# Performance work log

Hardware: AMD Instinct MI355X
Metric: run time of the kernel (lower is better)

The kernel has to match this reference:

```python
import jax, jax.numpy as jnp
import numpy as np


def setup_inputs() -> dict:
    key = jax.random.key(0)
    ks = jax.random.split(key, 10)
    N, CZ, CH = 512, 128, 128
    s = 1.0 / np.sqrt(CZ)  # keep pre-sigmoid activations in a sane range
    return {
        "z": jax.random.normal(ks[0], (N, N, CZ), dtype=jnp.float32),
        "mask": jnp.ones((N, N, 1), dtype=jnp.float32),
        "weight_ag": jax.random.normal(ks[1], (CH, CZ), dtype=jnp.float32) * s,
        "bias_ag": jax.random.normal(ks[2], (CH,), dtype=jnp.float32) * 0.02,
        "weight_ap": jax.random.normal(ks[3], (CH, CZ), dtype=jnp.float32) * s,
        "bias_ap": jax.random.normal(ks[4], (CH,), dtype=jnp.float32) * 0.02,
        "weight_bg": jax.random.normal(ks[5], (CH, CZ), dtype=jnp.float32) * s,
        "bias_bg": jax.random.normal(ks[6], (CH,), dtype=jnp.float32) * 0.02,
        "weight_bp": jax.random.normal(ks[7], (CH, CZ), dtype=jnp.float32) * s,
        "bias_bp": jax.random.normal(ks[8], (CH,), dtype=jnp.float32) * 0.02,
        "chunk_size": 32,
    }


def _triangle_mul(z, mask, w_ag, b_ag, w_ap, b_ap, w_bg, b_bg, w_bp, b_bp):
    # z: [N, N, c_z]; mask: [N, N, 1]; weights: [c, c_z]
    # a = mask * sigmoid(Linear_ag(z)) * Linear_ap(z)   -> [N, N, c]
    a = mask * jax.nn.sigmoid(jnp.einsum("ijz,cz->ijc", z, w_ag) + b_ag) * (
        jnp.einsum("ijz,cz->ijc", z, w_ap) + b_ap
    )
    b = mask * jax.nn.sigmoid(jnp.einsum("ijz,cz->ijc", z, w_bg) + b_bg) * (
        jnp.einsum("ijz,cz->ijc", z, w_bp) + b_bp
    )
    # outgoing triangle multiplicative combination, channel-first output [c, N, N]
    return jnp.einsum("ikc,jkc->cij", a, b)


def reference(z, mask, weight_ag, bias_ag, weight_ap, bias_ap,
              weight_bg, bias_bg, weight_bp, bias_bp, chunk_size):
    # The torch wrapper chunks the hidden-channel dim of the weights and
    # concatenates the per-chunk [c, N, N] outputs along dim 0. Since every
    # channel is independent, this is mathematically identical to running the
    # full computation at once; we do that (clean, fused form).
    return _triangle_mul(z, mask, weight_ag, bias_ag, weight_ap, bias_ap,
                         weight_bg, bias_bg, weight_bp, bias_bp)
```

## Files before the change

kernel.cpp:

```cpp
#include <hip/hip_runtime.h>
#include <stdint.h>


#define NDIM 512
#define CZ   128
#define CH   128
#define NPOS (NDIM * NDIM)
#define TILES 4

typedef __attribute__((ext_vector_type(8))) __bf16 bf16x8;
typedef __attribute__((ext_vector_type(4))) float  f32x4;

__device__ __forceinline__ unsigned short f2bf(float f) {
  unsigned int u = __builtin_bit_cast(unsigned int, f);
  unsigned int r = (u + 0x7fffu + ((u >> 16) & 1u)) >> 16;
  return (unsigned short)r;
}

__global__ __launch_bounds__(256) void conv_weights(
    const float* __restrict__ wag, const float* __restrict__ wap,
    const float* __restrict__ wbg, const float* __restrict__ wbp,
    unsigned short* __restrict__ wbf) {
  int idx = blockIdx.x * 256 + threadIdx.x;
  int proj = idx >> 14;
  int rem  = idx & 16383;
  const float* src = (proj == 0) ? wag : (proj == 1) ? wap : (proj == 2) ? wbg : wbp;
  wbf[idx] = f2bf(src[rem]);
}

__global__ __launch_bounds__(256, 2) void proj_fuse(
    const float* __restrict__ z,
    const float* __restrict__ mask,
    const unsigned short* __restrict__ wbf,
    const float* __restrict__ bias_ag, const float* __restrict__ bias_ap,
    const float* __restrict__ bias_bg, const float* __restrict__ bias_bp,
    unsigned short* __restrict__ a_ws,
    unsigned short* __restrict__ b_ws) {
  __shared__ unsigned short zbuf[64 * 136];
  __shared__ unsigned short tbuf[128 * 72];

  const int t    = threadIdx.x;
  const int lane = t & 63;
  const int wave = t >> 6;
  const int wm   = wave >> 1;
  const int wn   = wave & 1;
  const int pair = blockIdx.y;
  const int pg   = pair * 2, pp = pg + 1;

  const int mrow  = wm * 32 + (lane & 15);
  const int nrow  = wn * 64 + (lane & 15);
  const int koffl = (lane >> 4) * 8;

  bf16x8 wg[4][4], wp[4][4];
#pragma unroll
  for (int ks = 0; ks < 4; ++ks)
#pragma unroll
    for (int ni = 0; ni < 4; ++ni) {
      const int c = nrow + ni * 16;
      wg[ks][ni] = *(const bf16x8*)&wbf[(pg * CH + c) * CZ + ks * 32 + koffl];
      wp[ks][ni] = *(const bf16x8*)&wbf[(pp * CH + c) * CZ + ks * 32 + koffl];
    }

  const float* bgp = pair ? bias_bg : bias_ag;
  const float* bpp = pair ? bias_bp : bias_ap;
  unsigned short* plane = pair ? b_ws : a_ws;

  const int col4  = t & 31;
  const int rbase = t >> 5;

  const int m0 = blockIdx.x * (TILES * 64);

  float4 zf[8];
#pragma unroll
  for (int it = 0; it < 8; ++it)
    zf[it] = *(const float4*)(z + (size_t)(m0 + it * 8 + rbase) * CZ + col4 * 4);

  for (int tt = 0; tt < TILES; ++tt) {
    const int mt = m0 + tt * 64;

#pragma unroll
    for (int it = 0; it < 8; ++it) {
      const int row = it * 8 + rbase;
      unsigned int lo = (unsigned int)f2bf(zf[it].x) | ((unsigned int)f2bf(zf[it].y) << 16);
      unsigned int hi = (unsigned int)f2bf(zf[it].z) | ((unsigned int)f2bf(zf[it].w) << 16);
      *(uint2*)&zbuf[row * 136 + col4 * 4] = make_uint2(lo, hi);
    }
    __syncthreads();

    if (tt + 1 < TILES) {
#pragma unroll
      for (int it = 0; it < 8; ++it)
        zf[it] = *(const float4*)(z + (size_t)(mt + 64 + it * 8 + rbase) * CZ + col4 * 4);
    }
    float mk[2][4];
#pragma unroll
    for (int mi = 0; mi < 2; ++mi)
#pragma unroll
      for (int r = 0; r < 4; ++r)
        mk[mi][r] = mask[mt + wm * 32 + mi * 16 + (lane >> 4) * 4 + r];

    f32x4 accg[2][4], accp[2][4];
#pragma unroll
    for (int mi = 0; mi < 2; ++mi)
#pragma unroll
      for (int ni = 0; ni < 4; ++ni) {
        accg[mi][ni] = (f32x4){0.f, 0.f, 0.f, 0.f};
        accp[mi][ni] = (f32x4){0.f, 0.f, 0.f, 0.f};
      }
#pragma unroll
    for (int ks = 0; ks < 4; ++ks) {
      bf16x8 af0 = *(const bf16x8*)&zbuf[(mrow)      * 136 + ks * 32 + koffl];
      bf16x8 af1 = *(const bf16x8*)&zbuf[(mrow + 16) * 136 + ks * 32 + koffl];
#pragma unroll
      for (int ni = 0; ni < 4; ++ni) {
        accg[0][ni] = __builtin_amdgcn_mfma_f32_16x16x32_bf16(af0, wg[ks][ni], accg[0][ni], 0, 0, 0);
        accg[1][ni] = __builtin_amdgcn_mfma_f32_16x16x32_bf16(af1, wg[ks][ni], accg[1][ni], 0, 0, 0);
        accp[0][ni] = __builtin_amdgcn_mfma_f32_16x16x32_bf16(af0, wp[ks][ni], accp[0][ni], 0, 0, 0);
        accp[1][ni] = __builtin_amdgcn_mfma_f32_16x16x32_bf16(af1, wp[ks][ni], accp[1][ni], 0, 0, 0);
      }
    }

#pragma unroll
    for (int ni = 0; ni < 4; ++ni) {
      const int c = nrow + ni * 16;
      const float bgv = bgp[c];
      const float bpv = bpp[c];
#pragma unroll
      for (int mi = 0; mi < 2; ++mi) {
        unsigned short h[4];
#pragma unroll
        for (int r = 0; r < 4; ++r) {
          float g = accg[mi][ni][r] + bgv;
          float p = accp[mi][ni][r] + bpv;
          float s = 1.0f / (1.0f + __expf(-g));
          h[r] = f2bf(mk[mi][r] * s * p);
        }
        const int mloc = wm * 32 + mi * 16 + (lane >> 4) * 4;
        *(uint2*)&tbuf[c * 72 + mloc] =
            make_uint2((unsigned int)h[0] | ((unsigned int)h[1] << 16),
                       (unsigned int)h[2] | ((unsigned int)h[3] << 16));
      }
    }
    __syncthreads();

    {
      const int p4 = t & 15;
      const int cb = t >> 4;
#pragma unroll
      for (int it = 0; it < 8; ++it) {
        const int c = it * 16 + cb;
        uint2 v = *(const uint2*)&tbuf[c * 72 + p4 * 4];
        *(uint2*)(plane + (size_t)c * NPOS + mt + p4 * 4) = v;
      }
    }
  }
}

__global__ __launch_bounds__(256, 3) void tri_gemm(
    const unsigned short* __restrict__ a_ws,
    const unsigned short* __restrict__ b_ws,
    float* __restrict__ out) {
  __shared__ unsigned short sA[128 * 64];
  __shared__ unsigned short sB[128 * 64];

  const int t = threadIdx.x, lane = t & 63, wave = t >> 6;
  const int wm = wave >> 1, wn = wave & 1;
  const int tj = blockIdx.x, ti = blockIdx.y, c = blockIdx.z;
  const int i0 = ti * 128, j0 = tj * 128;

  const unsigned short* Ap = a_ws + (size_t)c * NPOS + (size_t)i0 * NDIM;
  const unsigned short* Bp = b_ws + (size_t)c * NPOS + (size_t)j0 * NDIM;

  f32x4 acc[4][4];
#pragma unroll
  for (int mi = 0; mi < 4; ++mi)
#pragma unroll
    for (int ni = 0; ni < 4; ++ni) acc[mi][ni] = (f32x4){0.f, 0.f, 0.f, 0.f};

  const int srow8  = t >> 3;
  const int schunk = t & 7;
  const int mrow = wm * 64 + (lane & 15);
  const int nrow = wn * 64 + (lane & 15);

  for (int kk = 0; kk < 8; ++kk) {
    const int k0 = kk * 64;
#pragma unroll
    for (int i = 0; i < 4; ++i) {
      const int row = i * 32 + srow8;
      const int kcs = schunk ^ (row & 7);
      __builtin_amdgcn_global_load_lds(
          (const __attribute__((address_space(1))) unsigned int*)(Ap + (size_t)row * NDIM + k0 + kcs * 8),
          (__attribute__((address_space(3))) unsigned int*)&sA[(i * 256 + t) * 8], 16, 0, 0);
      __builtin_amdgcn_global_load_lds(
          (const __attribute__((address_space(1))) unsigned int*)(Bp + (size_t)row * NDIM + k0 + kcs * 8),
          (__attribute__((address_space(3))) unsigned int*)&sB[(i * 256 + t) * 8], 16, 0, 0);
    }
    __syncthreads();

#pragma unroll
    for (int ksub = 0; ksub < 2; ++ksub) {
      const int kc = ksub * 4 + (lane >> 4);
      bf16x8 af[4], bfr[4];
#pragma unroll
      for (int mi = 0; mi < 4; ++mi) {
        const int r = mrow + mi * 16;
        af[mi] = *(const bf16x8*)&sA[r * 64 + ((kc ^ (r & 7)) << 3)];
      }
#pragma unroll
      for (int ni = 0; ni < 4; ++ni) {
        const int r = nrow + ni * 16;
        bfr[ni] = *(const bf16x8*)&sB[r * 64 + ((kc ^ (r & 7)) << 3)];
      }
#pragma unroll
      for (int mi = 0; mi < 4; ++mi)
#pragma unroll
        for (int ni = 0; ni < 4; ++ni)
          acc[mi][ni] = __builtin_amdgcn_mfma_f32_16x16x32_bf16(af[mi], bfr[ni], acc[mi][ni], 0, 0, 0);
    }
    __syncthreads();
  }

  float* O = out + (size_t)c * NPOS + (size_t)i0 * NDIM + j0;
#pragma unroll
  for (int mi = 0; mi < 4; ++mi)
#pragma unroll
    for (int r = 0; r < 4; ++r) {
      const int m = wm * 64 + mi * 16 + (lane >> 4) * 4 + r;
#pragma unroll
      for (int ni = 0; ni < 4; ++ni) {
        const int n = wn * 64 + ni * 16 + (lane & 15);
        O[(size_t)m * NDIM + n] = acc[mi][ni][r];
      }
    }
}

extern "C" void kernel_launch(void* const* d_in, const int* in_sizes, int n_in,
                              void* d_out, int out_size, void* d_ws, size_t ws_size,
                              hipStream_t stream) {
  const float* z    = (const float*)d_in[0];
  const float* mask = (const float*)d_in[1];
  const float* wag  = (const float*)d_in[2];
  const float* bag  = (const float*)d_in[3];
  const float* wap  = (const float*)d_in[4];
  const float* bap  = (const float*)d_in[5];
  const float* wbg  = (const float*)d_in[6];
  const float* bbg  = (const float*)d_in[7];
  const float* wbp  = (const float*)d_in[8];
  const float* bbp  = (const float*)d_in[9];
  float* out = (float*)d_out;

  unsigned short* wbf  = (unsigned short*)d_ws;
  unsigned short* a_ws = (unsigned short*)((char*)d_ws + 131072);
  unsigned short* b_ws = (unsigned short*)((char*)d_ws + 131072 + (size_t)CH * NPOS * 2);

  conv_weights<<<dim3(256), dim3(256), 0, stream>>>(wag, wap, wbg, wbp, wbf);
  proj_fuse<<<dim3(NPOS / (64 * TILES), 2), dim3(256), 0, stream>>>(
      z, mask, wbf, bag, bap, bbg, bbp, a_ws, b_ws);
  tri_gemm<<<dim3(4, 4, CH), dim3(256), 0, stream>>>(a_ws, b_ws, out);
}
```

Before: 435.0 us.

## Restructure projection kernel: one block computes all four projections for 32 positions

```diff
diff --git a/kernel.cpp b/kernel.cpp
--- a/kernel.cpp
+++ b/kernel.cpp
@@ -6,7 +6,6 @@
 #define CZ   128
 #define CH   128
 #define NPOS (NDIM * NDIM)
-#define TILES 4
 
 typedef __attribute__((ext_vector_type(8))) __bf16 bf16x8;
 typedef __attribute__((ext_vector_type(4))) float  f32x4;
@@ -15,6 +14,12 @@
   unsigned int u = __builtin_bit_cast(unsigned int, f);
   unsigned int r = (u + 0x7fffu + ((u >> 16) & 1u)) >> 16;
   return (unsigned short)r;
+}
+__device__ __forceinline__ float bf2f_lo(unsigned int u) {
+  return __builtin_bit_cast(float, u << 16);
+}
+__device__ __forceinline__ float bf2f_hi(unsigned int u) {
+  return __builtin_bit_cast(float, u & 0xffff0000u);
 }
 
 __global__ __launch_bounds__(256) void conv_weights(
@@ -28,7 +33,7 @@
   wbf[idx] = f2bf(src[rem]);
 }
 
-__global__ __launch_bounds__(256, 2) void proj_fuse(
+__global__ __launch_bounds__(256, 3) void proj_fuse(
     const float* __restrict__ z,
     const float* __restrict__ mask,
     const unsigned short* __restrict__ wbf,
@@ -36,122 +41,95 @@
     const float* __restrict__ bias_bg, const float* __restrict__ bias_bp,
     unsigned short* __restrict__ a_ws,
     unsigned short* __restrict__ b_ws) {
-  __shared__ unsigned short zbuf[64 * 136];
-  __shared__ unsigned short tbuf[128 * 72];
+  __shared__ unsigned short zbuf[32 * 136];
+  __shared__ unsigned short accb[4 * 128 * 36];
 
   const int t    = threadIdx.x;
   const int lane = t & 63;
-  const int wave = t >> 6;
-  const int wm   = wave >> 1;
-  const int wn   = wave & 1;
-  const int pair = blockIdx.y;
-  const int pg   = pair * 2, pp = pg + 1;
-
-  const int mrow  = wm * 32 + (lane & 15);
-  const int nrow  = wn * 64 + (lane & 15);
-  const int koffl = (lane >> 4) * 8;
-
-  bf16x8 wg[4][4], wp[4][4];
-#pragma unroll
-  for (int ks = 0; ks < 4; ++ks)
-#pragma unroll
-    for (int ni = 0; ni < 4; ++ni) {
-      const int c = nrow + ni * 16;
-      wg[ks][ni] = *(const bf16x8*)&wbf[(pg * CH + c) * CZ + ks * 32 + koffl];
-      wp[ks][ni] = *(const bf16x8*)&wbf[(pp * CH + c) * CZ + ks * 32 + koffl];
-    }
-
-  const float* bgp = pair ? bias_bg : bias_ag;
-  const float* bpp = pair ? bias_bp : bias_ap;
-  unsigned short* plane = pair ? b_ws : a_ws;
-
-  const int col4  = t & 31;
-  const int rbase = t >> 5;
-
-  const int m0 = blockIdx.x * (TILES * 64);
-
-  float4 zf[8];
-#pragma unroll
-  for (int it = 0; it < 8; ++it)
-    zf[it] = *(const float4*)(z + (size_t)(m0 + it * 8 + rbase) * CZ + col4 * 4);
-
-  for (int tt = 0; tt < TILES; ++tt) {
-    const int mt = m0 + tt * 64;
-
-#pragma unroll
-    for (int it = 0; it < 8; ++it) {
-      const int row = it * 8 + rbase;
-      unsigned int lo = (unsigned int)f2bf(zf[it].x) | ((unsigned int)f2bf(zf[it].y) << 16);
-      unsigned int hi = (unsigned int)f2bf(zf[it].z) | ((unsigned int)f2bf(zf[it].w) << 16);
-      *(uint2*)&zbuf[row * 136 + col4 * 4] = make_uint2(lo, hi);
-    }
-    __syncthreads();
-
-    if (tt + 1 < TILES) {
-#pragma unroll
-      for (int it = 0; it < 8; ++it)
-        zf[it] = *(const float4*)(z + (size_t)(mt + 64 + it * 8 + rbase) * CZ + col4 * 4);
-    }
-    float mk[2][4];
-#pragma unroll
-    for (int mi = 0; mi < 2; ++mi)
-#pragma unroll
-      for (int r = 0; r < 4; ++r)
-        mk[mi][r] = mask[mt + wm * 32 + mi * 16 + (lane >> 4) * 4 + r];
-
-    f32x4 accg[2][4], accp[2][4];
-#pragma unroll
-    for (int mi = 0; mi < 2; ++mi)
-#pragma unroll
-      for (int ni = 0; ni < 4; ++ni) {
-        accg[mi][ni] = (f32x4){0.f, 0.f, 0.f, 0.f};
-        accp[mi][ni] = (f32x4){0.f, 0.f, 0.f, 0.f};
-      }
-#pragma unroll
-    for (int ks = 0; ks < 4; ++ks) {
-      bf16x8 af0 = *(const bf16x8*)&zbuf[(mrow)      * 136 + ks * 32 + koffl];
-      bf16x8 af1 = *(const bf16x8*)&zbuf[(mrow + 16) * 136 + ks * 32 + koffl];
-#pragma unroll
-      for (int ni = 0; ni < 4; ++ni) {
-        accg[0][ni] = __builtin_amdgcn_mfma_f32_16x16x32_bf16(af0, wg[ks][ni], accg[0][ni], 0, 0, 0);
-        accg[1][ni] = __builtin_amdgcn_mfma_f32_16x16x32_bf16(af1, wg[ks][ni], accg[1][ni], 0, 0, 0);
-        accp[0][ni] = __builtin_amdgcn_mfma_f32_16x16x32_bf16(af0, wp[ks][ni], accp[0][ni], 0, 0, 0);
-        accp[1][ni] = __builtin_amdgcn_mfma_f32_16x16x32_bf16(af1, wp[ks][ni], accp[1][ni], 0, 0, 0);
-      }
-    }
-
-#pragma unroll
-    for (int ni = 0; ni < 4; ++ni) {
-      const int c = nrow + ni * 16;
-      const float bgv = bgp[c];
-      const float bpv = bpp[c];
-#pragma unroll
-      for (int mi = 0; mi < 2; ++mi) {
-        unsigned short h[4];
-#pragma unroll
-        for (int r = 0; r < 4; ++r) {
-          float g = accg[mi][ni][r] + bgv;
-          float p = accp[mi][ni][r] + bpv;
-          float s = 1.0f / (1.0f + __expf(-g));
-          h[r] = f2bf(mk[mi][r] * s * p);
-        }
-        const int mloc = wm * 32 + mi * 16 + (lane >> 4) * 4;
-        *(uint2*)&tbuf[c * 72 + mloc] =
-            make_uint2((unsigned int)h[0] | ((unsigned int)h[1] << 16),
-                       (unsigned int)h[2] | ((unsigned int)h[3] << 16));
-      }
-    }
-    __syncthreads();
-
-    {
-      const int p4 = t & 15;
-      const int cb = t >> 4;
-#pragma unroll
-      for (int it = 0; it < 8; ++it) {
-        const int c = it * 16 + cb;
-        uint2 v = *(const uint2*)&tbuf[c * 72 + p4 * 4];
-        *(uint2*)(plane + (size_t)c * NPOS + mt + p4 * 4) = v;
-      }
+  const int w    = t >> 6;
+  const int m0   = blockIdx.x * 32;
+
+  {
+    const int c4 = t & 31;
+    const int rb = t >> 5;
+#pragma unroll
+    for (int it = 0; it < 4; ++it) {
+      const int row = it * 8 + rb;
+      const float4 v = *(const float4*)(z + (size_t)(m0 + row) * CZ + c4 * 4);
+      unsigned int lo = (unsigned int)f2bf(v.x) | ((unsigned int)f2bf(v.y) << 16);
+      unsigned int hi = (unsigned int)f2bf(v.z) | ((unsigned int)f2bf(v.w) << 16);
+      *(uint2*)&zbuf[row * 136 + c4 * 4] = make_uint2(lo, hi);
+    }
+  }
+  __syncthreads();
+
+  const int ml    = lane & 15;
+  const int q     = lane >> 4;
+  const int koffl = q * 8;
+
+  f32x4 acc[2][8];
+#pragma unroll
+  for (int mi = 0; mi < 2; ++mi)
+#pragma unroll
+    for (int ni = 0; ni < 8; ++ni) acc[mi][ni] = (f32x4){0.f, 0.f, 0.f, 0.f};
+
+#pragma unroll
+  for (int ks = 0; ks < 4; ++ks) {
+    bf16x8 af0 = *(const bf16x8*)&zbuf[(ml)      * 136 + ks * 32 + koffl];
+    bf16x8 af1 = *(const bf16x8*)&zbuf[(ml + 16) * 136 + ks * 32 + koffl];
+#pragma unroll
+    for (int ni = 0; ni < 8; ++ni) {
+      bf16x8 wf = *(const bf16x8*)&wbf[((size_t)w * CH + ni * 16 + ml) * CZ + ks * 32 + koffl];
+      acc[0][ni] = __builtin_amdgcn_mfma_f32_16x16x32_bf16(af0, wf, acc[0][ni], 0, 0, 0);
+      acc[1][ni] = __builtin_amdgcn_mfma_f32_16x16x32_bf16(af1, wf, acc[1][ni], 0, 0, 0);
+    }
+  }
+
+#pragma unroll
+  for (int mi = 0; mi < 2; ++mi)
+#pragma unroll
+    for (int ni = 0; ni < 8; ++ni) {
+      const int c    = ni * 16 + ml;
+      const int pos0 = mi * 16 + q * 4;
+      unsigned int lo = (unsigned int)f2bf(acc[mi][ni][0]) |
+                        ((unsigned int)f2bf(acc[mi][ni][1]) << 16);
+      unsigned int hi = (unsigned int)f2bf(acc[mi][ni][2]) |
+                        ((unsigned int)f2bf(acc[mi][ni][3]) << 16);
+      *(uint2*)&accb[((size_t)w * CH + c) * 36 + pos0] = make_uint2(lo, hi);
+    }
+  __syncthreads();
+
+  const int pc = t & 7;
+  const int cb = t >> 3;
+  const float4 mv = *(const float4*)(mask + m0 + pc * 4);
+
+#pragma unroll
+  for (int pair = 0; pair < 2; ++pair) {
+    const float* bgp = pair ? bias_bg : bias_ag;
+    const float* bpp = pair ? bias_bp : bias_ap;
+    unsigned short* plane = pair ? b_ws : a_ws;
+    const int pg = pair * 2, pp = pg + 1;
+#pragma unroll
+    for (int it = 0; it < 4; ++it) {
+      const int ch = it * 32 + cb;
+      uint2 gv = *(const uint2*)&accb[((size_t)pg * CH + ch) * 36 + pc * 4];
+      uint2 pv = *(const uint2*)&accb[((size_t)pp * CH + ch) * 36 + pc * 4];
+      const float bg = bgp[ch];
+      const float bp = bpp[ch];
+      float g[4] = {bf2f_lo(gv.x) + bg, bf2f_hi(gv.x) + bg,
+                    bf2f_lo(gv.y) + bg, bf2f_hi(gv.y) + bg};
+      float p[4] = {bf2f_lo(pv.x) + bp, bf2f_hi(pv.x) + bp,
+                    bf2f_lo(pv.y) + bp, bf2f_hi(pv.y) + bp};
+      const float mr[4] = {mv.x, mv.y, mv.z, mv.w};
+      unsigned short h[4];
+#pragma unroll
+      for (int r = 0; r < 4; ++r) {
+        float s = 1.0f / (1.0f + __expf(-g[r]));
+        h[r] = f2bf(mr[r] * s * p[r]);
+      }
+      *(uint2*)(plane + (size_t)ch * NPOS + m0 + pc * 4) =
+          make_uint2((unsigned int)h[0] | ((unsigned int)h[1] << 16),
+                     (unsigned int)h[2] | ((unsigned int)h[3] << 16));
     }
   }
 }
@@ -254,7 +232,7 @@
   unsigned short* b_ws = (unsigned short*)((char*)d_ws + 131072 + (size_t)CH * NPOS * 2);
 
   conv_weights<<<dim3(256), dim3(256), 0, stream>>>(wag, wap, wbg, wbp, wbf);
-  proj_fuse<<<dim3(NPOS / (64 * TILES), 2), dim3(256), 0, stream>>>(
+  proj_fuse<<<dim3(NPOS / 32), dim3(256), 0, stream>>>(
       z, mask, wbf, bag, bap, bbg, bbp, a_ws, b_ws);
   tri_gemm<<<dim3(4, 4, CH), dim3(256), 0, stream>>>(a_ws, b_ws, out);
 }
```

Result: no change. 433.5 us (-0.4%).
